# Optimization experiments

Hardware: AMD Instinct MI355X
Metric: run time of the kernel (lower is better)

## Reference

```python
import jax, jax.numpy as jnp
import numpy as np

RADIUS = 1.0
BUMP = 32          # config.bump_steps
SCALE = 100.0      # sigmoid sharpness in compute_ecc
G = 32             # num_graphs

N, E, F = 16000, 48000, 32000
DIM, NDIR = 3, 64
HID, NC = 256, 10


def compute_ecc(h, index, lin):
    # h: [M, D]; lin: [BUMP] thresholds; index: [M] graph ids
    # sigmoid(scale * (lin - h)) broadcast -> [M, BUMP, D], segment-sum over M
    ecc = jax.nn.sigmoid(SCALE * (lin[None, :, None] - h[:, None, :]))
    return jax.ops.segment_sum(ecc, index, num_segments=G)  # [G, BUMP, D]


def setup_inputs() -> dict:
    key = jax.random.key(0)
    ks = jax.random.split(key, 12)
    x = jax.random.normal(ks[0], (N, DIM), dtype=jnp.float32)
    node_weights = jax.random.uniform(ks[1], (N,), dtype=jnp.float32)
    edge_weights = jax.random.uniform(ks[2], (E,), dtype=jnp.float32)
    face_weights = jax.random.uniform(ks[3], (F,), dtype=jnp.float32)
    v = jax.random.normal(ks[4], (DIM, NDIR), dtype=jnp.float32)
    v = v / jnp.linalg.norm(v, axis=0, keepdims=True)  # unit directions
    W1 = jax.random.normal(ks[5], (HID, NDIR * BUMP), dtype=jnp.float32) * 0.02
    b1 = jnp.zeros((HID,), dtype=jnp.float32)
    W2 = jax.random.normal(ks[6], (NC, HID), dtype=jnp.float32) * 0.02
    b2 = jnp.zeros((NC,), dtype=jnp.float32)
    edge_index = jax.random.randint(ks[7], (2, E), 0, N, dtype=jnp.int64)
    face = jax.random.randint(ks[8], (3, F), 0, N, dtype=jnp.int64)
    batch_ids = jnp.sort(jax.random.randint(ks[9], (N,), 0, G, dtype=jnp.int64))
    return {"x": x, "node_weights": node_weights, "edge_weights": edge_weights,
            "face_weights": face_weights, "v": v, "W1": W1, "b1": b1,
            "W2": W2, "b2": b2, "edge_index": edge_index, "face": face,
            "batch_ids": batch_ids}


def reference(x, node_weights, edge_weights, face_weights, v, W1, b1, W2, b2,
              edge_index, face, batch_ids):
    lin = jnp.linspace(-RADIUS, RADIUS, BUMP, dtype=jnp.float32)
    # node heights: weighted coords projected onto directions -> [N, D]
    nh = (x * node_weights[:, None]) @ v
    # edge heights: max over the 2 endpoints, then weight -> [E, D]
    eh = jnp.maximum(nh[edge_index[0]], nh[edge_index[1]]) * edge_weights[:, None]
    idx_e = batch_ids[edge_index[0]]
    # face heights: max over the 3 vertices -> [F, D]
    fh = jnp.max(nh[face], axis=0) * face_weights[:, None]
    idx_f = batch_ids[face[0]]
    ecc = compute_ecc(nh, batch_ids, lin)   # [G, BUMP, D]
    ecc = ecc - compute_ecc(eh, idx_e, lin)
    ecc = ecc + compute_ecc(fh, idx_f, lin)
    flat = ecc.reshape(G, -1)               # [G, BUMP*D]
    h = jax.nn.relu(flat @ W1.T + b1)
    logits = h @ W2.T + b2
    return (logits, flat)
```

## Files before the change

kernel.cpp:

```cpp
#include <hip/hip_runtime.h>
#include <hip/hip_bf16.h>

constexpr int NN = 16000, NE = 48000, NF = 32000;
constexpr int ND = 64, NB = 32, NG = 32;
constexpr int HIDN = 256, NCLS = 10;
constexpr int CHB = 32;
constexpr int EFB = (NE + NF + 255) / 256;
constexpr int PREB = (NN * ND) / 256;
constexpr int CAPE = 4096, CAPF = 4096;
constexpr float KLOG = 144.26950408889634f;
constexpr float DLT  = 9.307710457348151f;
constexpr float INV_DLT = 0.10743849569269015f;
constexpr int HBINS = 39;

struct alignas(8)  ERec { unsigned ab; float w; };
struct alignas(16) FRec { unsigned ab; unsigned c; float w; unsigned pad; };

constexpr int NH_OFF   = 0;
constexpr int ECCF_OFF = NH_OFF + NN * ND;
constexpr int CUR_OFF  = ECCF_OFF + NG * NB * ND;
constexpr int NOFS_OFF = CUR_OFF + 64;
constexpr int ER_OFF   = NOFS_OFF + 36;
constexpr int FR_OFF   = ER_OFF + NG * CAPE * 2;
constexpr int HB_OFF   = FR_OFF + NG * CAPF * 4;
constexpr int ZERO_CNT = NG * NB * ND;

__device__ __forceinline__ int clamp_node(int n) {
    return ((unsigned)n < (unsigned)NN) ? n : 0;
}
template<bool BF> __device__ __forceinline__ float ldf(const void* p, int i) {
    return BF ? __bfloat162float(((const __hip_bfloat16*)p)[i]) : ((const float*)p)[i];
}
template<bool I64> __device__ __forceinline__ int ldi(const int* p, int i) {
    return I64 ? p[2 * i] : p[i];
}

__device__ __forceinline__ bool detect_bf(const void* xp) {
    const unsigned* xw = (const unsigned*)xp;
    unsigned w = xw[threadIdx.x & 63];
    return __ballot(((w >> 23) & 0xFFu) >= 200u) != 0ull;
}
__device__ __forceinline__ bool detect_i64(const int* eip) {
    const unsigned* eiw = (const unsigned*)eip;
    unsigned o = eiw[2 * (threadIdx.x & 63) + 1];
    return __ballot(o != 0u) == 0ull;
}

__device__ __forceinline__ void accum_hist(float h, float s, float* hb) {
    const float KDEC = __builtin_amdgcn_exp2f(-DLT);
    float hkL = fmaf(h, KLOG, KLOG);
    float fl = floorf((hkL - 14.0f) * INV_DLT);
    int jlo = (int)fl + 1;
    if (jlo >= 32) return;
    if (jlo < -4) { hb[4 * 64] += s; return; }
    float t0 = fmaf(-(fl + 1.0f), DLT, hkL);
    float e  = __builtin_amdgcn_exp2f(t0);
    float s0 = __builtin_amdgcn_rcpf(1.0f + e);  e *= KDEC;
    float s1 = __builtin_amdgcn_rcpf(1.0f + e);  e *= KDEC;
    float s2 = __builtin_amdgcn_rcpf(1.0f + e);
    float* p = hb + (jlo + 4) * 64;
    float v0 = p[0], v1 = p[64], v2 = p[128], v3 = p[192];
    p[0]   = v0 + s * s0;
    p[64]  = v1 + s * (s1 - s0);
    p[128] = v2 + s * (s2 - s1);
    p[192] = v3 + s * (1.0f - s2);
}

template<bool BF, bool I64>
__device__ __forceinline__ void pre_body(const void* x, const void* nw, const void* v,
                                         const int* ei, const int* fc, const int* batch,
                                         const void* ew, const void* fw,
                                         float* wsf, int* wsi, unsigned* cur,
                                         ERec* er, FRec* fr,
                                         unsigned* cnt, unsigned* base) {
    int t = threadIdx.x;
    int gid = blockIdx.x * 256 + t;

    if (gid < ZERO_CNT) wsf[ECCF_OFF + gid] = 0.0f;

    if (gid < NN) {
        int gn = ldi<I64>(batch, gid) & (NG - 1);
        int gp = (gid > 0) ? (ldi<I64>(batch, gid - 1) & (NG - 1)) : -1;
        for (int gg = gp + 1; gg <= gn; gg++) wsi[NOFS_OFF + gg] = gid;
        if (gid == NN - 1)
            for (int gg = gn + 1; gg <= NG; gg++) wsi[NOFS_OFF + gg] = NN;
    }

    {
        int n = gid >> 6, d = gid & 63;
        float h = fmaf(ldf<BF>(x, n*3+2), ldf<BF>(v, 2*ND+d),
                  fmaf(ldf<BF>(x, n*3+1), ldf<BF>(v, ND+d),
                       ldf<BF>(x, n*3+0) * ldf<BF>(v, d))) * ldf<BF>(nw, n);
        wsf[NH_OFF + gid] = h;
    }

    if (blockIdx.x < EFB) {
        if (t < 64) cnt[t] = 0;
        __syncthreads();
        int id = blockIdx.x * 256 + t;
        int bin = 0; unsigned rank = 0; bool act = false;
        if (id < NE + NF) {
            if (id < NE) bin = ldi<I64>(batch, clamp_node(ldi<I64>(ei, id))) & 31;
            else bin = 32 + (ldi<I64>(batch, clamp_node(ldi<I64>(fc, id - NE))) & 31);
            act = true;
            rank = atomicAdd(&cnt[bin], 1u);
        }
        __syncthreads();
        if (t < 64) base[t] = cnt[t] ? atomicAdd(&cur[t], cnt[t]) : 0u;
        __syncthreads();
        if (act) {
            int off = (int)(base[bin] + rank);
            if (bin < 32) {
                if (off < CAPE) {
                    unsigned a = (unsigned)clamp_node(ldi<I64>(ei, id));
                    unsigned b = (unsigned)clamp_node(ldi<I64>(ei, NE + id));
                    ERec r; r.ab = a | (b << 14); r.w = ldf<BF>(ew, id);
                    er[bin * CAPE + off] = r;
                }
            } else {
                if (off < CAPF) {
                    int fid = id - NE;
                    unsigned a = (unsigned)clamp_node(ldi<I64>(fc, fid));
                    unsigned b = (unsigned)clamp_node(ldi<I64>(fc, NF + fid));
                    unsigned c = (unsigned)clamp_node(ldi<I64>(fc, 2 * NF + fid));
                    FRec r; r.ab = a | (b << 14); r.c = c;
                    r.w = ldf<BF>(fw, fid); r.pad = 0u;
                    fr[(bin - 32) * CAPF + off] = r;
                }
            }
        }
    }
}
__global__ __launch_bounds__(256) void k_pre(const void* __restrict__ x,
                                             const void* __restrict__ nw,
                                             const void* __restrict__ v,
                                             const int* __restrict__ ei,
                                             const int* __restrict__ fc,
                                             const int* __restrict__ batch,
                                             const void* __restrict__ ew,
                                             const void* __restrict__ fw,
                                             float* __restrict__ wsf,
                                             int* __restrict__ wsi,
                                             unsigned* __restrict__ cur,
                                             ERec* __restrict__ er,
                                             FRec* __restrict__ fr) {
    __shared__ unsigned cnt[64], base[64];
    bool bf = detect_bf(x), i64 = detect_i64(ei);
    if (bf)  { if (i64) pre_body<true,true >(x,nw,v,ei,fc,batch,ew,fw,wsf,wsi,cur,er,fr,cnt,base);
               else     pre_body<true,false>(x,nw,v,ei,fc,batch,ew,fw,wsf,wsi,cur,er,fr,cnt,base); }
    else     { if (i64) pre_body<false,true >(x,nw,v,ei,fc,batch,ew,fw,wsf,wsi,cur,er,fr,cnt,base);
               else     pre_body<false,false>(x,nw,v,ei,fc,batch,ew,fw,wsf,wsi,cur,er,fr,cnt,base); }
}

__global__ __launch_bounds__(256, 4) void k_ecc(const float* __restrict__ nh,
                                                const int* __restrict__ wsi,
                                                const unsigned* __restrict__ cur,
                                                float* __restrict__ eccf,
                                                const ERec* __restrict__ er,
                                                const FRec* __restrict__ fr) {
    __shared__ float hist[4 * HBINS * 64];
    int t = threadIdx.x;
    int d = t & 63;
    int w = __builtin_amdgcn_readfirstlane(t) >> 6;
    int g  = blockIdx.x >> 5;
    int cb = blockIdx.x & (CHB - 1);
    int sid = cb * 4 + w;
    const int S = CHB * 4;

    for (int j = t; j < 4 * HBINS * 64; j += 256) hist[j] = 0.0f;
    __syncthreads();

    float* hb = hist + w * (HBINS * 64) + d;

    int ns = wsi[NOFS_OFF + g], nend = wsi[NOFS_OFF + g + 1];
    int i = ns + sid;
    for (; i + 3 * S < nend; i += 4 * S) {
        float h1 = nh[i * ND + d];
        float h2 = nh[(i + S) * ND + d];
        float h3 = nh[(i + 2 * S) * ND + d];
        float h4 = nh[(i + 3 * S) * ND + d];
        accum_hist(h1, 1.0f, hb);
        accum_hist(h2, 1.0f, hb);
        accum_hist(h3, 1.0f, hb);
        accum_hist(h4, 1.0f, hb);
    }
    for (; i < nend; i += S) accum_hist(nh[i * ND + d], 1.0f, hb);

    int ecnt = min((int)cur[g], CAPE);
    const ERec* eg = er + g * CAPE;
    i = sid;
    if (i + 3 * S < ecnt) {
        ERec r1 = eg[i], r2 = eg[i + S], r3 = eg[i + 2 * S], r4 = eg[i + 3 * S];
        for (;;) {
            int ni = i + 4 * S;
            bool more = (ni + 3 * S < ecnt);
            float a1 = nh[(r1.ab & 16383) * ND + d], b1 = nh[((r1.ab >> 14) & 16383) * ND + d];
            float a2 = nh[(r2.ab & 16383) * ND + d], b2 = nh[((r2.ab >> 14) & 16383) * ND + d];
            float a3 = nh[(r3.ab & 16383) * ND + d], b3 = nh[((r3.ab >> 14) & 16383) * ND + d];
            float a4 = nh[(r4.ab & 16383) * ND + d], b4 = nh[((r4.ab >> 14) & 16383) * ND + d];
            ERec n1, n2, n3, n4;
            if (more) { n1 = eg[ni]; n2 = eg[ni + S]; n3 = eg[ni + 2 * S]; n4 = eg[ni + 3 * S]; }
            accum_hist(fmaxf(a1, b1) * r1.w, -1.0f, hb);
            accum_hist(fmaxf(a2, b2) * r2.w, -1.0f, hb);
            accum_hist(fmaxf(a3, b3) * r3.w, -1.0f, hb);
            accum_hist(fmaxf(a4, b4) * r4.w, -1.0f, hb);
            i = ni;
            if (!more) break;
            r1 = n1; r2 = n2; r3 = n3; r4 = n4;
        }
    }
    for (; i < ecnt; i += S) {
        ERec r = eg[i];
        float ha = nh[(r.ab & 16383) * ND + d], hbv = nh[((r.ab >> 14) & 16383) * ND + d];
        accum_hist(fmaxf(ha, hbv) * r.w, -1.0f, hb);
    }

    int fcnt = min((int)cur[32 + g], CAPF);
    const FRec* fg = fr + g * CAPF;
    i = sid;
    if (i + 3 * S < fcnt) {
        FRec r1 = fg[i], r2 = fg[i + S], r3 = fg[i + 2 * S], r4 = fg[i + 3 * S];
        for (;;) {
            int ni = i + 4 * S;
            bool more = (ni + 3 * S < fcnt);
            float a1 = nh[(r1.ab & 16383) * ND + d], b1 = nh[((r1.ab >> 14) & 16383) * ND + d];
            float c1 = nh[r1.c * ND + d];
            float a2 = nh[(r2.ab & 16383) * ND + d], b2 = nh[((r2.ab >> 14) & 16383) * ND + d];
            float c2 = nh[r2.c * ND + d];
            float a3 = nh[(r3.ab & 16383) * ND + d], b3 = nh[((r3.ab >> 14) & 16383) * ND + d];
            float c3 = nh[r3.c * ND + d];
            float a4 = nh[(r4.ab & 16383) * ND + d], b4 = nh[((r4.ab >> 14) & 16383) * ND + d];
            float c4 = nh[r4.c * ND + d];
            FRec n1, n2, n3, n4;
            if (more) { n1 = fg[ni]; n2 = fg[ni + S]; n3 = fg[ni + 2 * S]; n4 = fg[ni + 3 * S]; }
            accum_hist(fmaxf(fmaxf(a1, b1), c1) * r1.w, 1.0f, hb);
            accum_hist(fmaxf(fmaxf(a2, b2), c2) * r2.w, 1.0f, hb);
            accum_hist(fmaxf(fmaxf(a3, b3), c3) * r3.w, 1.0f, hb);
            accum_hist(fmaxf(fmaxf(a4, b4), c4) * r4.w, 1.0f, hb);
            i = ni;
            if (!more) break;
            r1 = n1; r2 = n2; r3 = n3; r4 = n4;
        }
    }
    for (; i < fcnt; i += S) {
        FRec r = fg[i];
        float ha = nh[(r.ab & 16383) * ND + d], hbv = nh[((r.ab >> 14) & 16383) * ND + d];
        float hc = nh[r.c * ND + d];
        accum_hist(fmaxf(fmaxf(ha, hbv), hc) * r.w, 1.0f, hb);
    }

    __syncthreads();
    for (int o = t; o < HBINS * 64; o += 256)
        hist[o] += hist[HBINS*64 + o] + hist[2*HBINS*64 + o] + hist[3*HBINS*64 + o];
    __syncthreads();
    if (t < 64) {
        float run = hist[t] + hist[64 + t] + hist[128 + t] + hist[192 + t];
        float* eb = eccf + g * (NB * ND) + t;
        for (int j = 0; j < 32; j++) {
            run += hist[(j + 4) * 64 + t];
            atomicAdd(eb + j * 64, run);
        }
    }
}

template<bool BF>
__device__ __forceinline__ void mlp1_body(const void* W1, const void* b1,
                                          const float* eccf, float* hbuf,
                                          void* outv, float* red, float* pr) {
    int g = blockIdx.x >> 3, hc = blockIdx.x & 7;
    int t = threadIdx.x;

    const float4* fp = (const float4*)(eccf + g * (NB * ND) + t * 8);
    float4 fa = fp[0], fb = fp[1];
    float fl[8] = {fa.x, fa.y, fa.z, fa.w, fb.x, fb.y, fb.z, fb.w};

    if (hc == 0) {
        int ob = NG * NCLS + g * (NB * ND) + t * 8;
        if (BF) {
#pragma unroll
            for (int j = 0; j < 8; j++)
                ((__hip_bfloat16*)outv)[ob + j] = __float2bfloat16(fl[j]);
        } else {
            ((float4*)((float*)outv + ob))[0] = fa;
            ((float4*)((float*)outv + ob))[1] = fb;
        }
    }

    float acc[32];
#pragma unroll
    for (int r = 0; r < 32; r++) acc[r] = 0.0f;
#pragma unroll 4
    for (int r = 0; r < 32; r++) {
        size_t wb = (size_t)(hc * 32 + r) * (NB * ND) + t * 8;
        float wv[8];
        if (BF) {
            uint4 u = *(const uint4*)((const __hip_bfloat16*)W1 + wb);
            wv[0] = __uint_as_float(u.x << 16); wv[1] = __uint_as_float(u.x & 0xffff0000u);
            wv[2] = __uint_as_float(u.y << 16); wv[3] = __uint_as_float(u.y & 0xffff0000u);
            wv[4] = __uint_as_float(u.z << 16); wv[5] = __uint_as_float(u.z & 0xffff0000u);
            wv[6] = __uint_as_float(u.w << 16); wv[7] = __uint_as_float(u.w & 0xffff0000u);
        } else {
            float4 a = *(const float4*)((const float*)W1 + wb);
            float4 b = *(const float4*)((const float*)W1 + wb + 4);
            wv[0]=a.x; wv[1]=a.y; wv[2]=a.z; wv[3]=a.w;
            wv[4]=b.x; wv[5]=b.y; wv[6]=b.z; wv[7]=b.w;
        }
        float s = 0.0f;
#pragma unroll
        for (int j = 0; j < 8; j++) s = fmaf(wv[j], fl[j], s);
        acc[r] = s;
    }

#pragma unroll
    for (int r = 0; r < 32; r++) red[t * 33 + r] = acc[r];
    __syncthreads();
    {
        int r = t >> 3, s8 = t & 7;
        float sum = 0.0f;
#pragma unroll
        for (int i = 0; i < 32; i++) sum += red[(s8 * 32 + i) * 33 + r];
        pr[r * 8 + s8] = sum;
    }
    __syncthreads();
    if (t < 32) {
        float h = ldf<BF>(b1, hc * 32 + t);
#pragma unroll
        for (int s8 = 0; s8 < 8; s8++) h += pr[t * 8 + s8];
        hbuf[g * HIDN + hc * 32 + t] = fmaxf(h, 0.0f);
    }
}
__global__ __launch_bounds__(256) void k_mlp1(const void* __restrict__ W1,
                                              const void* __restrict__ b1,
                                              const float* __restrict__ eccf,
                                              float* __restrict__ hbuf,
                                              void* __restrict__ outv,
                                              const void* __restrict__ x) {
    __shared__ float red[256 * 33];
    __shared__ float pr[256];
    if (detect_bf(x)) mlp1_body<true>(W1, b1, eccf, hbuf, outv, red, pr);
    else              mlp1_body<false>(W1, b1, eccf, hbuf, outv, red, pr);
}

template<bool BF>
__device__ __forceinline__ void mlp2_body(const void* W2, const void* b2,
                                          const float* hbuf, void* outv, float* hs) {
    int g = blockIdx.x, t = threadIdx.x;
    hs[t] = hbuf[g * HIDN + t];
    __syncthreads();
    int w = t >> 6, lane = t & 63;
    for (int c = w; c < NCLS; c += 4) {
        float p = hs[lane]        * ldf<BF>(W2, c * HIDN + lane)
                + hs[lane + 64]   * ldf<BF>(W2, c * HIDN + lane + 64)
                + hs[lane + 128]  * ldf<BF>(W2, c * HIDN + lane + 128)
                + hs[lane + 192]  * ldf<BF>(W2, c * HIDN + lane + 192);
#pragma unroll
        for (int off = 32; off >= 1; off >>= 1) p += __shfl_xor(p, off);
        if (lane == 0) {
            float r = p + ldf<BF>(b2, c);
            if (BF) ((__hip_bfloat16*)outv)[g * NCLS + c] = __float2bfloat16(r);
            else    ((float*)outv)[g * NCLS + c] = r;
        }
    }
}
__global__ __launch_bounds__(256) void k_mlp2(const void* __restrict__ W2,
                                              const void* __restrict__ b2,
                                              const float* __restrict__ hbuf,
                                              void* __restrict__ outv,
                                              const void* __restrict__ x) {
    __shared__ float hs[HIDN];
    if (detect_bf(x)) mlp2_body<true>(W2, b2, hbuf, outv, hs);
    else              mlp2_body<false>(W2, b2, hbuf, outv, hs);
}

extern "C" void kernel_launch(void* const* d_in, const int* in_sizes, int n_in,
                              void* d_out, int out_size, void* d_ws, size_t ws_size,
                              hipStream_t stream) {
    const void* x  = d_in[0];
    const void* nw = d_in[1];
    const void* ew = d_in[2];
    const void* fw = d_in[3];
    const void* v  = d_in[4];
    const void* W1 = d_in[5];
    const void* b1 = d_in[6];
    const void* W2 = d_in[7];
    const void* b2 = d_in[8];
    const int* ei    = (const int*)d_in[9];
    const int* fc    = (const int*)d_in[10];
    const int* batch = (const int*)d_in[11];

    float*    wsf = (float*)d_ws;
    unsigned* wsu = (unsigned*)d_ws;
    int*      wsi = (int*)d_ws;
    float*    nh   = wsf + NH_OFF;
    float*    eccf = wsf + ECCF_OFF;
    unsigned* cur  = wsu + CUR_OFF;
    float*    hbuf = wsf + HB_OFF;
    ERec*     er   = (ERec*)(wsf + ER_OFF);
    FRec*     fr   = (FRec*)(wsf + FR_OFF);

    hipMemsetAsync((char*)d_ws + (size_t)CUR_OFF * 4, 0, 64 * 4, stream);

    k_pre<<<PREB, 256, 0, stream>>>(x, nw, v, ei, fc, batch, ew, fw, wsf, wsi, cur, er, fr);
    k_ecc<<<NG * CHB, 256, 0, stream>>>(nh, wsi, cur, eccf, er, fr);
    k_mlp1<<<NG * 8, 256, 0, stream>>>(W1, b1, eccf, hbuf, d_out, x);
    k_mlp2<<<NG, 256, 0, stream>>>(W2, b2, hbuf, d_out, x);
}
```

Before: 121.1 us.

## Vectorize node heights, share LDS histogram via atomics, fuse MLP kernels

```diff
diff --git a/kernel.cpp b/kernel.cpp
--- a/kernel.cpp
+++ b/kernel.cpp
@@ -6,7 +6,7 @@
 constexpr int HIDN = 256, NCLS = 10;
 constexpr int CHB = 32;
 constexpr int EFB = (NE + NF + 255) / 256;
-constexpr int PREB = (NN * ND) / 256;
+constexpr int PREB = (NN * 16) / 256;
 constexpr int CAPE = 4096, CAPF = 4096;
 constexpr float KLOG = 144.26950408889634f;
 constexpr float DLT  = 9.307710457348151f;
@@ -20,7 +20,8 @@
 constexpr int ECCF_OFF = NH_OFF + NN * ND;
 constexpr int CUR_OFF  = ECCF_OFF + NG * NB * ND;
 constexpr int NOFS_OFF = CUR_OFF + 64;
-constexpr int ER_OFF   = NOFS_OFF + 36;
+constexpr int DONE_OFF = NOFS_OFF + 40;
+constexpr int ER_OFF   = DONE_OFF + 32;
 constexpr int FR_OFF   = ER_OFF + NG * CAPE * 2;
 constexpr int HB_OFF   = FR_OFF + NG * CAPF * 4;
 constexpr int ZERO_CNT = NG * NB * ND;
@@ -30,6 +31,18 @@
 }
 template<bool BF> __device__ __forceinline__ float ldf(const void* p, int i) {
     return BF ? __bfloat162float(((const __hip_bfloat16*)p)[i]) : ((const float*)p)[i];
+}
+template<bool BF> __device__ __forceinline__ float4 ldf4(const void* p, int i) {
+    if (BF) {
+        uint2 u = *(const uint2*)((const unsigned short*)p + i);
+        float4 r;
+        r.x = __uint_as_float((u.x & 0xffffu) << 16);
+        r.y = __uint_as_float(u.x & 0xffff0000u);
+        r.z = __uint_as_float((u.y & 0xffffu) << 16);
+        r.w = __uint_as_float(u.y & 0xffff0000u);
+        return r;
+    }
+    return *(const float4*)((const float*)p + i);
 }
 template<bool I64> __device__ __forceinline__ int ldi(const int* p, int i) {
     return I64 ? p[2 * i] : p[i];
@@ -52,18 +65,17 @@
     float fl = floorf((hkL - 14.0f) * INV_DLT);
     int jlo = (int)fl + 1;
     if (jlo >= 32) return;
-    if (jlo < -4) { hb[4 * 64] += s; return; }
+    if (jlo < -4) { atomicAdd(hb + 4 * 64, s); return; }
     float t0 = fmaf(-(fl + 1.0f), DLT, hkL);
     float e  = __builtin_amdgcn_exp2f(t0);
     float s0 = __builtin_amdgcn_rcpf(1.0f + e);  e *= KDEC;
     float s1 = __builtin_amdgcn_rcpf(1.0f + e);  e *= KDEC;
     float s2 = __builtin_amdgcn_rcpf(1.0f + e);
     float* p = hb + (jlo + 4) * 64;
-    float v0 = p[0], v1 = p[64], v2 = p[128], v3 = p[192];
-    p[0]   = v0 + s * s0;
-    p[64]  = v1 + s * (s1 - s0);
-    p[128] = v2 + s * (s2 - s1);
-    p[192] = v3 + s * (1.0f - s2);
+    atomicAdd(p,       s * s0);
+    atomicAdd(p + 64,  s * (s1 - s0));
+    atomicAdd(p + 128, s * (s2 - s1));
+    atomicAdd(p + 192, s * (1.0f - s2));
 }
 
 template<bool BF, bool I64>
@@ -76,7 +88,13 @@
     int t = threadIdx.x;
     int gid = blockIdx.x * 256 + t;
 
-    if (gid < ZERO_CNT) wsf[ECCF_OFF + gid] = 0.0f;
+    if (gid < ZERO_CNT / 4) {
+        float4 z; z.x = z.y = z.z = z.w = 0.0f;
+        *(float4*)(wsf + ECCF_OFF + gid * 4) = z;
+    }
+
+    if (blockIdx.x == PREB - 1 && t < 32)
+        ((unsigned*)wsi)[DONE_OFF + t] = 0u;
 
     if (gid < NN) {
         int gn = ldi<I64>(batch, gid) & (NG - 1);
@@ -87,11 +105,18 @@
     }
 
     {
-        int n = gid >> 6, d = gid & 63;
-        float h = fmaf(ldf<BF>(x, n*3+2), ldf<BF>(v, 2*ND+d),
-                  fmaf(ldf<BF>(x, n*3+1), ldf<BF>(v, ND+d),
-                       ldf<BF>(x, n*3+0) * ldf<BF>(v, d))) * ldf<BF>(nw, n);
-        wsf[NH_OFF + gid] = h;
+        int n = gid >> 4, d0 = (gid & 15) * 4;
+        float x0 = ldf<BF>(x, n * 3 + 0), x1 = ldf<BF>(x, n * 3 + 1);
+        float x2 = ldf<BF>(x, n * 3 + 2), wn = ldf<BF>(nw, n);
+        float4 v0 = ldf4<BF>(v, d0);
+        float4 v1 = ldf4<BF>(v, ND + d0);
+        float4 v2 = ldf4<BF>(v, 2 * ND + d0);
+        float4 h;
+        h.x = fmaf(x2, v2.x, fmaf(x1, v1.x, x0 * v0.x)) * wn;
+        h.y = fmaf(x2, v2.y, fmaf(x1, v1.y, x0 * v0.y)) * wn;
+        h.z = fmaf(x2, v2.z, fmaf(x1, v1.z, x0 * v0.z)) * wn;
+        h.w = fmaf(x2, v2.w, fmaf(x1, v1.w, x0 * v0.w)) * wn;
+        *(float4*)(wsf + NH_OFF + n * ND + d0) = h;
     }
 
     if (blockIdx.x < EFB) {
@@ -158,19 +183,21 @@
                                                 float* __restrict__ eccf,
                                                 const ERec* __restrict__ er,
                                                 const FRec* __restrict__ fr) {
-    __shared__ float hist[4 * HBINS * 64];
+    __shared__ float hist[HBINS * 64];
+    __shared__ float segw[256];
     int t = threadIdx.x;
     int d = t & 63;
     int w = __builtin_amdgcn_readfirstlane(t) >> 6;
-    int g  = blockIdx.x >> 5;
-    int cb = blockIdx.x & (CHB - 1);
+    int p = blockIdx.x;
+    int g  = ((p & 7) << 2) | ((p >> 8) & 3);
+    int cb = (p >> 3) & (CHB - 1);
     int sid = cb * 4 + w;
     const int S = CHB * 4;
 
-    for (int j = t; j < 4 * HBINS * 64; j += 256) hist[j] = 0.0f;
-    __syncthreads();
-
-    float* hb = hist + w * (HBINS * 64) + d;
+    for (int j = t; j < HBINS * 64; j += 256) hist[j] = 0.0f;
+    __syncthreads();
+
+    float* hb = hist + d;
 
     int ns = wsi[NOFS_OFF + g], nend = wsi[NOFS_OFF + g + 1];
     int i = ns + sid;
@@ -250,23 +277,31 @@
     }
 
     __syncthreads();
-    for (int o = t; o < HBINS * 64; o += 256)
-        hist[o] += hist[HBINS*64 + o] + hist[2*HBINS*64 + o] + hist[3*HBINS*64 + o];
-    __syncthreads();
-    if (t < 64) {
-        float run = hist[t] + hist[64 + t] + hist[128 + t] + hist[192 + t];
-        float* eb = eccf + g * (NB * ND) + t;
-        for (int j = 0; j < 32; j++) {
-            run += hist[(j + 4) * 64 + t];
-            atomicAdd(eb + j * 64, run);
-        }
+    {
+        float run = 0.0f, pre[8];
+#pragma unroll
+        for (int jj = 0; jj < 8; jj++) {
+            run += hist[(4 + w * 8 + jj) * 64 + d];
+            pre[jj] = run;
+        }
+        segw[w * 64 + d] = run;
+        float padb = hist[d] + hist[64 + d] + hist[128 + d] + hist[192 + d];
+        __syncthreads();
+        float base = padb;
+        for (int u = 0; u < 3; u++) if (u < w) base += segw[u * 64 + d];
+        float* eb = eccf + g * (NB * ND) + d;
+#pragma unroll
+        for (int jj = 0; jj < 8; jj++)
+            unsafeAtomicAdd(eb + (w * 8 + jj) * 64, base + pre[jj]);
     }
 }
 
 template<bool BF>
-__device__ __forceinline__ void mlp1_body(const void* W1, const void* b1,
-                                          const float* eccf, float* hbuf,
-                                          void* outv, float* red, float* pr) {
+__device__ __forceinline__ void mlp_body(const void* W1, const void* b1,
+                                         const void* W2, const void* b2,
+                                         const float* eccf, float* hbuf,
+                                         unsigned* done, void* outv,
+                                         float* red, float* pr, unsigned* lastflag) {
     int g = blockIdx.x >> 3, hc = blockIdx.x & 7;
     int t = threadIdx.x;
 
@@ -328,48 +363,47 @@
         for (int s8 = 0; s8 < 8; s8++) h += pr[t * 8 + s8];
         hbuf[g * HIDN + hc * 32 + t] = fmaxf(h, 0.0f);
     }
-}
-__global__ __launch_bounds__(256) void k_mlp1(const void* __restrict__ W1,
-                                              const void* __restrict__ b1,
-                                              const float* __restrict__ eccf,
-                                              float* __restrict__ hbuf,
-                                              void* __restrict__ outv,
-                                              const void* __restrict__ x) {
+
+    __syncthreads();
+    if (t == 0) {
+        __threadfence();
+        *lastflag = (atomicAdd(&done[g], 1u) == 7u) ? 1u : 0u;
+    }
+    __syncthreads();
+    if (*lastflag) {
+        __threadfence();
+        red[t] = hbuf[g * HIDN + t];
+        __syncthreads();
+        int w = t >> 6, lane = t & 63;
+        for (int c = w; c < NCLS; c += 4) {
+            float p = red[lane]        * ldf<BF>(W2, c * HIDN + lane)
+                    + red[lane + 64]   * ldf<BF>(W2, c * HIDN + lane + 64)
+                    + red[lane + 128]  * ldf<BF>(W2, c * HIDN + lane + 128)
+                    + red[lane + 192]  * ldf<BF>(W2, c * HIDN + lane + 192);
+#pragma unroll
+            for (int off = 32; off >= 1; off >>= 1) p += __shfl_xor(p, off);
+            if (lane == 0) {
+                float r = p + ldf<BF>(b2, c);
+                if (BF) ((__hip_bfloat16*)outv)[g * NCLS + c] = __float2bfloat16(r);
+                else    ((float*)outv)[g * NCLS + c] = r;
+            }
+        }
+    }
+}
+__global__ __launch_bounds__(256) void k_mlp(const void* __restrict__ W1,
+                                             const void* __restrict__ b1,
+                                             const void* __restrict__ W2,
+                                             const void* __restrict__ b2,
+                                             const float* __restrict__ eccf,
+                                             float* __restrict__ hbuf,
+                                             unsigned* __restrict__ done,
+                                             void* __restrict__ outv,
+                                             const void* __restrict__ x) {
     __shared__ float red[256 * 33];
     __shared__ float pr[256];
-    if (detect_bf(x)) mlp1_body<true>(W1, b1, eccf, hbuf, outv, red, pr);
-    else              mlp1_body<false>(W1, b1, eccf, hbuf, outv, red, pr);
-}
-
-template<bool BF>
-__device__ __forceinline__ void mlp2_body(const void* W2, const void* b2,
-                                          const float* hbuf, void* outv, float* hs) {
-    int g = blockIdx.x, t = threadIdx.x;
-    hs[t] = hbuf[g * HIDN + t];
-    __syncthreads();
-    int w = t >> 6, lane = t & 63;
-    for (int c = w; c < NCLS; c += 4) {
-        float p = hs[lane]        * ldf<BF>(W2, c * HIDN + lane)
-                + hs[lane + 64]   * ldf<BF>(W2, c * HIDN + lane + 64)
-                + hs[lane + 128]  * ldf<BF>(W2, c * HIDN + lane + 128)
-                + hs[lane + 192]  * ldf<BF>(W2, c * HIDN + lane + 192);
-#pragma unroll
-        for (int off = 32; off >= 1; off >>= 1) p += __shfl_xor(p, off);
-        if (lane == 0) {
-            float r = p + ldf<BF>(b2, c);
-            if (BF) ((__hip_bfloat16*)outv)[g * NCLS + c] = __float2bfloat16(r);
-            else    ((float*)outv)[g * NCLS + c] = r;
-        }
-    }
-}
-__global__ __launch_bounds__(256) void k_mlp2(const void* __restrict__ W2,
-                                              const void* __restrict__ b2,
-                                              const float* __restrict__ hbuf,
-                                              void* __restrict__ outv,
-                                              const void* __restrict__ x) {
-    __shared__ float hs[HIDN];
-    if (detect_bf(x)) mlp2_body<true>(W2, b2, hbuf, outv, hs);
-    else              mlp2_body<false>(W2, b2, hbuf, outv, hs);
+    __shared__ unsigned lastflag;
+    if (detect_bf(x)) mlp_body<true >(W1, b1, W2, b2, eccf, hbuf, done, outv, red, pr, &lastflag);
+    else              mlp_body<false>(W1, b1, W2, b2, eccf, hbuf, done, outv, red, pr, &lastflag);
 }
 
 extern "C" void kernel_launch(void* const* d_in, const int* in_sizes, int n_in,
@@ -394,6 +428,7 @@
     float*    nh   = wsf + NH_OFF;
     float*    eccf = wsf + ECCF_OFF;
     unsigned* cur  = wsu + CUR_OFF;
+    unsigned* done = wsu + DONE_OFF;
     float*    hbuf = wsf + HB_OFF;
     ERec*     er   = (ERec*)(wsf + ER_OFF);
     FRec*     fr   = (FRec*)(wsf + FR_OFF);
@@ -402,6 +437,5 @@
 
     k_pre<<<PREB, 256, 0, stream>>>(x, nw, v, ei, fc, batch, ew, fw, wsf, wsi, cur, er, fr);
     k_ecc<<<NG * CHB, 256, 0, stream>>>(nh, wsi, cur, eccf, er, fr);
-    k_mlp1<<<NG * 8, 256, 0, stream>>>(W1, b1, eccf, hbuf, d_out, x);
-    k_mlp2<<<NG, 256, 0, stream>>>(W2, b2, hbuf, d_out, x);
-}
+    k_mlp<<<NG * 8, 256, 0, stream>>>(W1, b1, W2, b2, eccf, hbuf, done, d_out, x);
+}
```

New measurement: 250.4 us. 107% more time.
